# Optimization experiments

Hardware: AMD Instinct MI355X
Metric: run time of the kernel (lower is better)

Reference implementation:

```python
import jax, jax.numpy as jnp
import numpy as np
from jax import lax

EPS = 1e-5

def _conv(x, w, stride=1, pad=0, groups=1):
    return lax.conv_general_dilated(
        x, w, (stride, stride), ((pad, pad), (pad, pad)),
        dimension_numbers=('NCHW', 'OIHW', 'NCHW'),
        feature_group_count=groups)

def _bn(x, gamma, beta):
    # BatchNorm2d, training-mode batch statistics (biased variance)
    mean = jnp.mean(x, axis=(0, 2, 3), keepdims=True)
    var = jnp.var(x, axis=(0, 2, 3), keepdims=True)
    xn = (x - mean) * lax.rsqrt(var + EPS)
    return xn * gamma[None, :, None, None] + beta[None, :, None, None]

def _silu(x):
    return x * jax.nn.sigmoid(x)

def setup_inputs() -> dict:
    key = jax.random.key(0)
    ks = jax.random.split(key, 20)
    B, C, H, W = 16, 128, 128, 128
    L2 = 100
    s = 0.05
    d = {
        'x': jax.random.normal(ks[0], (B, C, H, W), jnp.float32),
        'dce_output': jax.random.normal(ks[1], (B, L2, C), jnp.float32),
        # per-channel 3x3 convs fused as one depthwise conv [C,1,3,3]
        'dw_conv': jax.random.normal(ks[2], (C, 1, 3, 3), jnp.float32) * s,
        'W_dce1': jax.random.normal(ks[3], (L2 * C, C), jnp.float32) * s,
        'b_dce1': jnp.zeros((C,), jnp.float32),
        'W_dce2': jax.random.normal(ks[4], (C, C), jnp.float32) * s,
        'b_dce2': jnp.zeros((C,), jnp.float32),
        'W_sh': jax.random.normal(ks[5], (C, C // 2), jnp.float32) * s,
        'b_sh': jnp.zeros((C // 2,), jnp.float32),
        'W_ex': jax.random.normal(ks[6], (C // 2, C), jnp.float32) * s,
        'b_ex': jnp.zeros((C,), jnp.float32),
        'conv1_w': jax.random.normal(ks[7], (C, C, 3, 3), jnp.float32) * s,
        'bn1_g': jnp.ones((C,), jnp.float32),
        'bn1_b': jnp.zeros((C,), jnp.float32),
        'conv2_w': jax.random.normal(ks[8], (C, C, 1, 1), jnp.float32) * s,
        'bn2_g': jnp.ones((C,), jnp.float32),
        'bn2_b': jnp.zeros((C,), jnp.float32),
        'sc_w': jax.random.normal(ks[9], (C, C, 1, 1), jnp.float32) * s,
        'bnsc_g': jnp.ones((C,), jnp.float32),
        'bnsc_b': jnp.zeros((C,), jnp.float32),
    }
    return d

def reference(x, dce_output, dw_conv, W_dce1, b_dce1, W_dce2, b_dce2,
              W_sh, b_sh, W_ex, b_ex, conv1_w, bn1_g, bn1_b,
              conv2_w, bn2_g, bn2_b, sc_w, bnsc_g, bnsc_b):
    B, C, H, W = x.shape
    stride = 1
    # DCE FFN: Linear -> GELU(exact) -> Linear
    dce_flat = dce_output.reshape(B, -1)
    h = jax.nn.gelu(dce_flat @ W_dce1 + b_dce1, approximate=False)
    dce_features = h @ W_dce2 + b_dce2  # [B, C]
    # per-channel 3x3 conv + global avg pool, fused as depthwise conv
    sp = _conv(x, dw_conv, stride=1, pad=1, groups=C)
    spatial_features = jnp.mean(sp, axis=(2, 3))  # [B, C]
    # SE-style modulation
    m = dce_features * spatial_features
    shrunk = jax.nn.gelu(m @ W_sh + b_sh, approximate=False)
    mod_w = jax.nn.sigmoid(shrunk @ W_ex + b_ex)  # [B, C]
    xm = x * mod_w[:, :, None, None]
    # ResBlock
    bb = _bn(_conv(xm, conv1_w, stride=stride, pad=1), bn1_g, bn1_b)
    bb = _silu(bb)
    bb = _bn(_conv(bb, conv2_w, stride=1, pad=0), bn2_g, bn2_b)
    sc = _bn(_conv(xm, sc_w, stride=stride, pad=0), bnsc_g, bnsc_b)
    return _silu(bb + sc)
```

## Files before the change

kernel.cpp:

```cpp
#include <hip/hip_runtime.h>
#include <hip/hip_bf16.h>

typedef _Float16 f16;
typedef __attribute__((ext_vector_type(8))) _Float16 f16x8;
typedef __attribute__((ext_vector_type(4))) _Float16 f16x4;
typedef __attribute__((ext_vector_type(4))) float f32x4;

__device__ __forceinline__ float geluf(float x) {
    return 0.5f * x * (1.0f + erff(x * 0.70710678118654752440f));
}
__device__ __forceinline__ float sigmf(float x) { return 1.0f / (1.0f + __expf(-x)); }

#define NB 16
#define NC 128
#define NH 128
#define NW 128
#define PLANE (NH * NW)
#define NSTAT 262144.0f

__device__ __align__(16) f16 g_Wc[9 * 4 * 128 * 32];
__device__ __align__(16) f16 g_Wsc[4 * 128 * 32];
__device__ __align__(16) f16 g_W2[4 * 128 * 32];
__device__ __align__(16) f16 g_xmT[(size_t)16 * 128 * 4 * 130 * 32];
__device__ __align__(16) f16 g_y1T[(size_t)16 * 128 * 4 * 128 * 32];
__device__ __align__(16) f16 g_bbT[(size_t)16 * 128 * 4 * 128 * 32];

__global__ __launch_bounds__(256) void k_wprep(const float* __restrict__ c1w,
                                               const float* __restrict__ scw,
                                               const float* __restrict__ c2w) {
    int i = blockIdx.x * 256 + threadIdx.x;
    if (i < 147456) {
        int tap = i / 16384;
        int rem = i - tap * 16384;
        int chunk = rem >> 12;
        int r2 = rem & 4095;
        int co = r2 >> 5;
        int cil = r2 & 31;
        int ci = chunk * 32 + cil;
        g_Wc[i] = (f16)c1w[((size_t)co * 128 + ci) * 9 + tap];
    } else if (i < 163840) {
        int j = i - 147456;
        int chunk = j >> 12;
        int r2 = j & 4095;
        int co = r2 >> 5;
        int cil = r2 & 31;
        g_Wsc[j] = (f16)scw[(size_t)co * 128 + chunk * 32 + cil];
    } else if (i < 180224) {
        int j = i - 163840;
        int chunk = j >> 12;
        int r2 = j & 4095;
        int co = r2 >> 5;
        int cil = j & 31;
        g_W2[j] = (f16)c2w[(size_t)co * 128 + chunk * 32 + cil];
    }
}

__global__ __launch_bounds__(256) void k_dce1(const float* __restrict__ dce,
                                              const float* __restrict__ W1,
                                              float* __restrict__ dh) {
    int ks = blockIdx.x;
    int kbase = ks * 100;
    int t = threadIdx.x;
    __shared__ float sdce[16][100];
    for (int e = t; e < 1600; e += 256) {
        int bb = e / 100, k = e - bb * 100;
        sdce[bb][k] = dce[(size_t)bb * 12800 + kbase + k];
    }
    __syncthreads();
    int j = t & 127;
    int bg = t >> 7;
    float accs[8];
#pragma unroll
    for (int i = 0; i < 8; ++i) accs[i] = 0.0f;
    for (int k = 0; k < 100; ++k) {
        float wv = W1[((size_t)(kbase + k)) * 128 + j];
#pragma unroll
        for (int bb = 0; bb < 8; ++bb) accs[bb] += sdce[bg * 8 + bb][k] * wv;
    }
#pragma unroll
    for (int bb = 0; bb < 8; ++bb)
        atomicAdd(&dh[(bg * 8 + bb) * 128 + j], accs[bb]);
}

__global__ __launch_bounds__(128) void k_dce2(const float* __restrict__ dh,
                                              const float* __restrict__ b1,
                                              const float* __restrict__ W2,
                                              const float* __restrict__ b2,
                                              float* __restrict__ feat) {
    int b = blockIdx.x, j = threadIdx.x;
    __shared__ float sh[128];
    sh[j] = geluf(dh[b * 128 + j] + b1[j]);
    __syncthreads();
    float acc = b2[j];
    for (int k = 0; k < 128; ++k) acc += sh[k] * W2[k * 128 + j];
    feat[b * 128 + j] = acc;
}

__global__ __launch_bounds__(256) void k_spatial(const float* __restrict__ x,
                                                 const float* __restrict__ dw,
                                                 float* __restrict__ spat) {
    int bc = blockIdx.x;
    int t = threadIdx.x;
    const float* p = x + (size_t)bc * PLANE;
    float f = 0, r0 = 0, r1 = 0, c0 = 0, c1 = 0;
    for (int i = t; i < PLANE; i += 256) {
        float v = p[i];
        int row = i >> 7, col = i & 127;
        f += v;
        if (row == 0) r0 += v;
        if (row == 127) r1 += v;
        if (col == 0) c0 += v;
        if (col == 127) c1 += v;
    }
#pragma unroll
    for (int o = 1; o < 64; o <<= 1) {
        f  += __shfl_xor(f, o);
        r0 += __shfl_xor(r0, o);
        r1 += __shfl_xor(r1, o);
        c0 += __shfl_xor(c0, o);
        c1 += __shfl_xor(c1, o);
    }
    __shared__ float wr[4][5];
    int wid = t >> 6;
    if ((t & 63) == 0) {
        wr[wid][0] = f; wr[wid][1] = r0; wr[wid][2] = r1; wr[wid][3] = c0; wr[wid][4] = c1;
    }
    __syncthreads();
    if (t == 0) {
        float full = 0, row0 = 0, row127 = 0, col0 = 0, col127 = 0;
#pragma unroll
        for (int w = 0; w < 4; ++w) {
            full += wr[w][0]; row0 += wr[w][1]; row127 += wr[w][2];
            col0 += wr[w][3]; col127 += wr[w][4];
        }
        int c = bc & 127;
        float x00 = p[0];
        float x0e = p[127];
        float xe0 = p[127 * 128];
        float xee = p[127 * 128 + 127];
        float acc = 0.0f;
        for (int kh = 0; kh < 3; ++kh)
            for (int kw = 0; kw < 3; ++kw) {
                int dh_ = kh - 1, dwv = kw - 1;
                float T = full;
                if (dh_ == -1) T -= row127;
                else if (dh_ == 1) T -= row0;
                if (dwv == -1) T -= col127;
                else if (dwv == 1) T -= col0;
                if (dh_ == -1 && dwv == -1) T += xee;
                if (dh_ == -1 && dwv == 1) T += xe0;
                if (dh_ == 1 && dwv == -1) T += x0e;
                if (dh_ == 1 && dwv == 1) T += x00;
                acc += dw[c * 9 + kh * 3 + kw] * T;
            }
        spat[bc] = acc * (1.0f / 16384.0f);
    }
}

__global__ __launch_bounds__(128) void k_mod(const float* __restrict__ feat,
                                             const float* __restrict__ spat,
                                             const float* __restrict__ Wsh,
                                             const float* __restrict__ bsh,
                                             const float* __restrict__ Wex,
                                             const float* __restrict__ bex,
                                             float* __restrict__ mod) {
    int b = blockIdx.x, t = threadIdx.x;
    __shared__ float sm[128], ssh[64];
    sm[t] = feat[b * 128 + t] * spat[b * 128 + t];
    __syncthreads();
    if (t < 64) {
        float acc = bsh[t];
        for (int c = 0; c < 128; ++c) acc += sm[c] * Wsh[c * 64 + t];
        ssh[t] = geluf(acc);
    }
    __syncthreads();
    float acc = bex[t];
    for (int k = 0; k < 64; ++k) acc += ssh[k] * Wex[k * 128 + t];
    mod[b * 128 + t] = sigmf(acc);
}

__global__ __launch_bounds__(256) void k_xprep(const float* __restrict__ x,
                                               const float* __restrict__ mod) {
    int bid = blockIdx.x;
    int h = bid & 127;
    int b = bid >> 7;
    int t = threadIdx.x;
    __shared__ float sx[32][133];

    for (int chunk = 0; chunk < 4; ++chunk) {
        __syncthreads();
#pragma unroll
        for (int it = 0; it < 4; ++it) {
            int ci = it * 8 + (t >> 5);
            int w4 = t & 31;
            int cig = chunk * 32 + ci;
            float4 v = *(const float4*)&x[(((size_t)b * 128 + cig) * 128 + h) * 128 + w4 * 4];
            float m = mod[b * 128 + cig];
            sx[ci][w4 * 4 + 0] = v.x * m;
            sx[ci][w4 * 4 + 1] = v.y * m;
            sx[ci][w4 * 4 + 2] = v.z * m;
            sx[ci][w4 * 4 + 3] = v.w * m;
        }
        __syncthreads();
        f16* dstc = g_xmT + (((size_t)(b * 128 + h)) * 4 + chunk) * 4160;
        for (int g = t; g < 520; g += 256) {
            int s = g >> 2, c8 = g & 3;
            f16x8 o;
            if (s == 0 || s == 129) {
#pragma unroll
                for (int j = 0; j < 8; ++j) o[j] = (f16)0.f;
            } else {
#pragma unroll
                for (int j = 0; j < 8; ++j) o[j] = (f16)sx[c8 * 8 + j][s - 1];
            }
            *(f16x8*)(dstc + s * 32 + c8 * 8) = o;
        }
    }
}

__global__ __launch_bounds__(256, 3) void k_conv1m(float* __restrict__ stats) {
    int orig = blockIdx.x;
    int sw = (orig & 7) * 256 + (orig >> 3);
    int h = sw & 127;
    int b = sw >> 7;
    int t = threadIdx.x;
    int lane = t & 63;
    int wv = t >> 6;
    int l15 = lane & 15, lg = lane >> 4;
    int co_half = (wv >> 1) * 64;
    int w_half = (wv & 1) * 64;

    f32x4 acc[4][4];
#pragma unroll
    for (int ct = 0; ct < 4; ++ct)
#pragma unroll
        for (int wt = 0; wt < 4; ++wt) acc[ct][wt] = (f32x4){0.f, 0.f, 0.f, 0.f};

    f16x8 z8;
#pragma unroll
    for (int j = 0; j < 8; ++j) z8[j] = (f16)0.f;

    const f16* xrow[3];
    bool rok[3];
#pragma unroll
    for (int r = 0; r < 3; ++r) {
        int hr = h + r - 1;
        rok[r] = ((unsigned)hr < 128u);
        xrow[r] = g_xmT + ((size_t)(b * 128 + (rok[r] ? hr : 0))) * 4 * 4160;
    }

#pragma unroll
    for (int chunk = 0; chunk < 4; ++chunk) {
#pragma unroll
        for (int tap = 0; tap < 9; ++tap) {
            const int kh = tap / 3, kw = tap - kh * 3;
            f16x8 af[4], bf[4];
#pragma unroll
            for (int ct = 0; ct < 4; ++ct)
                af[ct] = *(const f16x8*)(g_Wc + ((size_t)(tap * 4 + chunk) * 128 + co_half + ct * 16 + l15) * 32 + lg * 8);
            if (rok[kh]) {
#pragma unroll
                for (int wt = 0; wt < 4; ++wt)
                    bf[wt] = *(const f16x8*)(xrow[kh] + (size_t)chunk * 4160
                                             + (w_half + wt * 16 + l15 + kw) * 32 + lg * 8);
            } else {
#pragma unroll
                for (int wt = 0; wt < 4; ++wt) bf[wt] = z8;
            }
#pragma unroll
            for (int ct = 0; ct < 4; ++ct)
#pragma unroll
                for (int wt = 0; wt < 4; ++wt)
                    acc[ct][wt] = __builtin_amdgcn_mfma_f32_16x16x32_f16(
                        af[ct], bf[wt], acc[ct][wt], 0, 0, 0);
        }
    }

#pragma unroll
    for (int ct = 0; ct < 4; ++ct) {
        int cog = (wv >> 1) * 2 + (ct >> 1);
        int col = (ct & 1) * 16 + lg * 4;
#pragma unroll
        for (int wt = 0; wt < 4; ++wt) {
            int w = w_half + wt * 16 + l15;
            f16x4 pk;
            pk[0] = (f16)acc[ct][wt][0];
            pk[1] = (f16)acc[ct][wt][1];
            pk[2] = (f16)acc[ct][wt][2];
            pk[3] = (f16)acc[ct][wt][3];
            *(f16x4*)(g_y1T + ((((size_t)(b * 128 + h)) * 4 + cog) * 128 + w) * 32 + col) = pk;
        }
#pragma unroll
        for (int r = 0; r < 4; ++r) {
            int co = co_half + ct * 16 + lg * 4 + r;
            float s = 0, q = 0;
#pragma unroll
            for (int wt = 0; wt < 4; ++wt) {
                float v = acc[ct][wt][r];
                s += v; q += v * v;
            }
#pragma unroll
            for (int o = 1; o < 16; o <<= 1) {
                s += __shfl_xor(s, o);
                q += __shfl_xor(q, o);
            }
            if (l15 == 0) {
                atomicAdd(&stats[co], s);
                atomicAdd(&stats[128 + co], q);
            }
        }
    }
}

__global__ __launch_bounds__(128) void k_fin1(const float* __restrict__ stats,
                                              const float* __restrict__ g1, const float* __restrict__ be1,
                                              float* __restrict__ coef) {
    int t = threadIdx.x;
    const float inv = 1.0f / NSTAT;
    float m = stats[t] * inv;
    float v = stats[128 + t] * inv - m * m;
    float a = g1[t] * rsqrtf(v + 1e-5f);
    coef[t] = a;
    coef[128 + t] = be1[t] - m * a;
}

__global__ __launch_bounds__(256, 2) void k_conv2m(const float* __restrict__ coef,
                                                   float* __restrict__ stats) {
    int orig = blockIdx.x;
    int sw = (orig & 7) * 256 + (orig >> 3);
    int h = sw & 127;
    int b = sw >> 7;
    int t = threadIdx.x;
    int lane = t & 63;
    int wv = t >> 6;
    int l15 = lane & 15, lg = lane >> 4;
    int co_half = (wv >> 1) * 64;
    int w_half = (wv & 1) * 64;

    f32x4 acc[4][4], asc[4][4];
#pragma unroll
    for (int ct = 0; ct < 4; ++ct)
#pragma unroll
        for (int wt = 0; wt < 4; ++wt) {
            acc[ct][wt] = (f32x4){0.f, 0.f, 0.f, 0.f};
            asc[ct][wt] = (f32x4){0.f, 0.f, 0.f, 0.f};
        }

    for (int chunk = 0; chunk < 4; ++chunk) {
        float ca[8], cc[8];
#pragma unroll
        for (int j = 0; j < 8; ++j) {
            int ci = chunk * 32 + lg * 8 + j;
            ca[j] = coef[ci];
            cc[j] = coef[128 + ci];
        }
        f16x8 bfr[4], bx[4];
#pragma unroll
        for (int wt = 0; wt < 4; ++wt) {
            int w = w_half + wt * 16 + l15;
            f16x8 raw = *(const f16x8*)(g_y1T + ((((size_t)(b * 128 + h)) * 4 + chunk) * 128 + w) * 32 + lg * 8);
#pragma unroll
            for (int j = 0; j < 8; ++j) {
                float v = ca[j] * (float)raw[j] + cc[j];
                bfr[wt][j] = (f16)(v * sigmf(v));
            }
            bx[wt] = *(const f16x8*)(g_xmT + (((size_t)(b * 128 + h)) * 4 + chunk) * 4160 + (w + 1) * 32 + lg * 8);
        }
        if (wv < 2) {
#pragma unroll
            for (int wt = 0; wt < 4; ++wt) {
                int w = w_half + wt * 16 + l15;
                *(f16x8*)(g_bbT + ((((size_t)(b * 128 + h)) * 4 + chunk) * 128 + w) * 32 + lg * 8) = bfr[wt];
            }
        }
        f16x8 af[4], sf[4];
#pragma unroll
        for (int ct = 0; ct < 4; ++ct) {
            af[ct] = *(const f16x8*)(g_W2 + ((size_t)chunk * 128 + co_half + ct * 16 + l15) * 32 + lg * 8);
            sf[ct] = *(const f16x8*)(g_Wsc + ((size_t)chunk * 128 + co_half + ct * 16 + l15) * 32 + lg * 8);
        }
#pragma unroll
        for (int ct = 0; ct < 4; ++ct)
#pragma unroll
            for (int wt = 0; wt < 4; ++wt) {
                acc[ct][wt] = __builtin_amdgcn_mfma_f32_16x16x32_f16(
                    af[ct], bfr[wt], acc[ct][wt], 0, 0, 0);
                asc[ct][wt] = __builtin_amdgcn_mfma_f32_16x16x32_f16(
                    sf[ct], bx[wt], asc[ct][wt], 0, 0, 0);
            }
    }

#pragma unroll
    for (int ct = 0; ct < 4; ++ct) {
#pragma unroll
        for (int r = 0; r < 4; ++r) {
            int co = co_half + ct * 16 + lg * 4 + r;
            float s = 0, q = 0, ss = 0, qq = 0;
#pragma unroll
            for (int wt = 0; wt < 4; ++wt) {
                float v = acc[ct][wt][r];
                s += v; q += v * v;
                float u = asc[ct][wt][r];
                ss += u; qq += u * u;
            }
#pragma unroll
            for (int o = 1; o < 16; o <<= 1) {
                s += __shfl_xor(s, o);
                q += __shfl_xor(q, o);
                ss += __shfl_xor(ss, o);
                qq += __shfl_xor(qq, o);
            }
            if (l15 == 0) {
                atomicAdd(&stats[512 + co], s);
                atomicAdd(&stats[640 + co], q);
                atomicAdd(&stats[256 + co], ss);
                atomicAdd(&stats[384 + co], qq);
            }
        }
    }
}

__global__ __launch_bounds__(256) void k_fin2(const float* __restrict__ stats,
                                              const float* __restrict__ g2, const float* __restrict__ be2,
                                              const float* __restrict__ gsc, const float* __restrict__ bsc,
                                              float* __restrict__ coef) {
    int t = threadIdx.x;
    const float inv = 1.0f / NSTAT;
    if (t < 128) {
        float m = stats[512 + t] * inv;
        float v = stats[640 + t] * inv - m * m;
        float a = g2[t] * rsqrtf(v + 1e-5f);
        coef[512 + t] = a;
        coef[640 + t] = be2[t] - m * a;
    } else {
        int c = t - 128;
        float m = stats[256 + c] * inv;
        float v = stats[384 + c] * inv - m * m;
        float a = gsc[c] * rsqrtf(v + 1e-5f);
        coef[256 + c] = a;
        coef[384 + c] = bsc[c] - m * a;
    }
}

__global__ __launch_bounds__(256, 2) void k_final(float* __restrict__ out,
                                                  const float* __restrict__ coef) {
    int orig = blockIdx.x;
    int sw = (orig & 7) * 256 + (orig >> 3);
    int h = sw & 127;
    int b = sw >> 7;
    int t = threadIdx.x;
    int lane = t & 63;
    int wv = t >> 6;
    int l15 = lane & 15, lg = lane >> 4;
    int co_half = (wv >> 1) * 64;
    int w_half = (wv & 1) * 64;

    f32x4 acc[4][4], asc[4][4];
#pragma unroll
    for (int ct = 0; ct < 4; ++ct)
#pragma unroll
        for (int wt = 0; wt < 4; ++wt) {
            acc[ct][wt] = (f32x4){0.f, 0.f, 0.f, 0.f};
            asc[ct][wt] = (f32x4){0.f, 0.f, 0.f, 0.f};
        }

    for (int chunk = 0; chunk < 4; ++chunk) {
        f16x8 bf[4], bx[4], af[4], sf[4];
#pragma unroll
        for (int wt = 0; wt < 4; ++wt) {
            int w = w_half + wt * 16 + l15;
            bf[wt] = *(const f16x8*)(g_bbT + ((((size_t)(b * 128 + h)) * 4 + chunk) * 128 + w) * 32 + lg * 8);
            bx[wt] = *(const f16x8*)(g_xmT + (((size_t)(b * 128 + h)) * 4 + chunk) * 4160 + (w + 1) * 32 + lg * 8);
        }
#pragma unroll
        for (int ct = 0; ct < 4; ++ct) {
            af[ct] = *(const f16x8*)(g_W2 + ((size_t)chunk * 128 + co_half + ct * 16 + l15) * 32 + lg * 8);
            sf[ct] = *(const f16x8*)(g_Wsc + ((size_t)chunk * 128 + co_half + ct * 16 + l15) * 32 + lg * 8);
        }
#pragma unroll
        for (int ct = 0; ct < 4; ++ct)
#pragma unroll
            for (int wt = 0; wt < 4; ++wt) {
                acc[ct][wt] = __builtin_amdgcn_mfma_f32_16x16x32_f16(
                    af[ct], bf[wt], acc[ct][wt], 0, 0, 0);
                asc[ct][wt] = __builtin_amdgcn_mfma_f32_16x16x32_f16(
                    sf[ct], bx[wt], asc[ct][wt], 0, 0, 0);
            }
    }

#pragma unroll
    for (int ct = 0; ct < 4; ++ct) {
#pragma unroll
        for (int r = 0; r < 4; ++r) {
            int co = co_half + ct * 16 + lg * 4 + r;
            float a2 = coef[512 + co], c2 = coef[640 + co];
            float as = coef[256 + co], cs = coef[384 + co];
#pragma unroll
            for (int wt = 0; wt < 4; ++wt) {
                float v = a2 * acc[ct][wt][r] + c2 + as * asc[ct][wt][r] + cs;
                v = v * sigmf(v);
                out[(((size_t)b * 128 + co) * 128 + h) * 128 + w_half + wt * 16 + l15] = v;
            }
        }
    }
}

extern "C" void kernel_launch(void* const* d_in, const int* in_sizes, int n_in,
                              void* d_out, int out_size, void* d_ws, size_t ws_size,
                              hipStream_t stream) {
    (void)in_sizes; (void)n_in; (void)out_size; (void)ws_size;
    const float* x    = (const float*)d_in[0];
    const float* dce  = (const float*)d_in[1];
    const float* dwc  = (const float*)d_in[2];
    const float* W1   = (const float*)d_in[3];
    const float* b1   = (const float*)d_in[4];
    const float* W2d  = (const float*)d_in[5];
    const float* b2d  = (const float*)d_in[6];
    const float* Wsh  = (const float*)d_in[7];
    const float* bsh  = (const float*)d_in[8];
    const float* Wex  = (const float*)d_in[9];
    const float* bex  = (const float*)d_in[10];
    const float* c1w  = (const float*)d_in[11];
    const float* g1   = (const float*)d_in[12];
    const float* be1  = (const float*)d_in[13];
    const float* c2w  = (const float*)d_in[14];
    const float* g2   = (const float*)d_in[15];
    const float* be2  = (const float*)d_in[16];
    const float* scw  = (const float*)d_in[17];
    const float* gsc  = (const float*)d_in[18];
    const float* bsc  = (const float*)d_in[19];

    float* F = (float*)d_ws;
    float* dh    = F;
    float* stats = F + 2048;
    float* coef  = F + 2816;
    float* feat  = F + 3584;
    float* spat  = F + 5632;
    float* md    = F + 7680;

    float* out = (float*)d_out;

    hipMemsetAsync(F, 0, (2048 + 768) * sizeof(float), stream);

    k_wprep<<<704, 256, 0, stream>>>(c1w, scw, c2w);
    k_dce1<<<128, 256, 0, stream>>>(dce, W1, dh);
    k_dce2<<<16, 128, 0, stream>>>(dh, b1, W2d, b2d, feat);
    k_spatial<<<2048, 256, 0, stream>>>(x, dwc, spat);
    k_mod<<<16, 128, 0, stream>>>(feat, spat, Wsh, bsh, Wex, bex, md);
    k_xprep<<<2048, 256, 0, stream>>>(x, md);
    k_conv1m<<<2048, 256, 0, stream>>>(stats);
    k_fin1<<<1, 128, 0, stream>>>(stats, g1, be1, coef);
    k_conv2m<<<2048, 256, 0, stream>>>(coef, stats);
    k_fin2<<<1, 256, 0, stream>>>(stats, g2, be2, gsc, bsc, coef);
    k_final<<<2048, 256, 0, stream>>>(out, coef);
}
```

Baseline: 1.266 ms.

## Fold modulation into per-batch weights, fuse spatial stats into x transpose, LDS-stage conv1

The separate spatial-reduction pass over x is removed; k_xprep now accumulates the per-channel sums, border rows/columns and corners with atomics while it transposes unmodulated x to fp16. The channel modulation is folded into per-batch copies of the conv1 and shortcut weights (k_wmod), so x no longer needs a second modulated pass. conv1 stages its three input rows into double-buffered, swizzled LDS via global_load_lds instead of reading them directly from global memory. conv2 no longer writes bbT and the final kernel recomputes BN+SiLU from y1T, which removes one large intermediate write and read. In exchange there are more atomics, per-batch weight storage, and duplicated elementwise work.

New measurement: 1.288 ms. No clear change (+1.7%).

```diff
diff --git a/kernel.cpp b/kernel.cpp
--- a/kernel.cpp
+++ b/kernel.cpp
@@ -21,14 +21,19 @@
 __device__ __align__(16) f16 g_Wc[9 * 4 * 128 * 32];
 __device__ __align__(16) f16 g_Wsc[4 * 128 * 32];
 __device__ __align__(16) f16 g_W2[4 * 128 * 32];
-__device__ __align__(16) f16 g_xmT[(size_t)16 * 128 * 4 * 130 * 32];
+__device__ __align__(16) f16 g_Wcb[(size_t)16 * 9 * 4 * 128 * 32];
+__device__ __align__(16) f16 g_Wscb[(size_t)16 * 4 * 128 * 32];
+__device__ __align__(16) f16 g_xT[(size_t)16 * 128 * 4 * 130 * 32];
 __device__ __align__(16) f16 g_y1T[(size_t)16 * 128 * 4 * 128 * 32];
-__device__ __align__(16) f16 g_bbT[(size_t)16 * 128 * 4 * 128 * 32];
+__device__ __align__(16) f16 g_zrow[4160];
+__device__ float g_red[5][16][128];
+__device__ float g_corn[4][16][128];
 
 __global__ __launch_bounds__(256) void k_wprep(const float* __restrict__ c1w,
                                                const float* __restrict__ scw,
                                                const float* __restrict__ c2w) {
     int i = blockIdx.x * 256 + threadIdx.x;
+    if (i < 10240) ((float*)g_red)[i] = 0.0f;
     if (i < 147456) {
         int tap = i / 16384;
         int rem = i - tap * 16384;
@@ -96,50 +101,77 @@
     feat[b * 128 + j] = acc;
 }
 
-__global__ __launch_bounds__(256) void k_spatial(const float* __restrict__ x,
-                                                 const float* __restrict__ dw,
-                                                 float* __restrict__ spat) {
-    int bc = blockIdx.x;
-    int t = threadIdx.x;
-    const float* p = x + (size_t)bc * PLANE;
-    float f = 0, r0 = 0, r1 = 0, c0 = 0, c1 = 0;
-    for (int i = t; i < PLANE; i += 256) {
-        float v = p[i];
-        int row = i >> 7, col = i & 127;
-        f += v;
-        if (row == 0) r0 += v;
-        if (row == 127) r1 += v;
-        if (col == 0) c0 += v;
-        if (col == 127) c1 += v;
-    }
-#pragma unroll
-    for (int o = 1; o < 64; o <<= 1) {
-        f  += __shfl_xor(f, o);
-        r0 += __shfl_xor(r0, o);
-        r1 += __shfl_xor(r1, o);
-        c0 += __shfl_xor(c0, o);
-        c1 += __shfl_xor(c1, o);
-    }
-    __shared__ float wr[4][5];
-    int wid = t >> 6;
-    if ((t & 63) == 0) {
-        wr[wid][0] = f; wr[wid][1] = r0; wr[wid][2] = r1; wr[wid][3] = c0; wr[wid][4] = c1;
-    }
-    __syncthreads();
-    if (t == 0) {
-        float full = 0, row0 = 0, row127 = 0, col0 = 0, col127 = 0;
-#pragma unroll
-        for (int w = 0; w < 4; ++w) {
-            full += wr[w][0]; row0 += wr[w][1]; row127 += wr[w][2];
-            col0 += wr[w][3]; col127 += wr[w][4];
-        }
-        int c = bc & 127;
-        float x00 = p[0];
-        float x0e = p[127];
-        float xe0 = p[127 * 128];
-        float xee = p[127 * 128 + 127];
+__global__ __launch_bounds__(256) void k_xprep(const float* __restrict__ x) {
+    int bid = blockIdx.x;
+    int h = bid & 127;
+    int b = bid >> 7;
+    int t = threadIdx.x;
+    int w4 = t & 31;
+    __shared__ float sx[32][133];
+
+    for (int chunk = 0; chunk < 4; ++chunk) {
+        __syncthreads();
+#pragma unroll
+        for (int it = 0; it < 4; ++it) {
+            int ci = it * 8 + (t >> 5);
+            int cig = chunk * 32 + ci;
+            float4 v = *(const float4*)&x[(((size_t)b * 128 + cig) * 128 + h) * 128 + w4 * 4];
+            sx[ci][w4 * 4 + 0] = v.x;
+            sx[ci][w4 * 4 + 1] = v.y;
+            sx[ci][w4 * 4 + 2] = v.z;
+            sx[ci][w4 * 4 + 3] = v.w;
+            float s4 = v.x + v.y + v.z + v.w;
+#pragma unroll
+            for (int o = 1; o < 32; o <<= 1) s4 += __shfl_xor(s4, o);
+            if (w4 == 0) {
+                atomicAdd(&g_red[0][b][cig], s4);
+                if (h == 0) atomicAdd(&g_red[1][b][cig], s4);
+                if (h == 127) atomicAdd(&g_red[2][b][cig], s4);
+                atomicAdd(&g_red[3][b][cig], v.x);
+                if (h == 0) g_corn[0][b][cig] = v.x;
+                if (h == 127) g_corn[2][b][cig] = v.x;
+            }
+            if (w4 == 31) {
+                atomicAdd(&g_red[4][b][cig], v.w);
+                if (h == 0) g_corn[1][b][cig] = v.w;
+                if (h == 127) g_corn[3][b][cig] = v.w;
+            }
+        }
+        __syncthreads();
+        f16* dstc = g_xT + (((size_t)(b * 128 + h)) * 4 + chunk) * 4160;
+        for (int g = t; g < 520; g += 256) {
+            int s = g >> 2, c8 = g & 3;
+            f16x8 o;
+            if (s == 0 || s == 129) {
+#pragma unroll
+                for (int j = 0; j < 8; ++j) o[j] = (f16)0.f;
+            } else {
+#pragma unroll
+                for (int j = 0; j < 8; ++j) o[j] = (f16)sx[c8 * 8 + j][s - 1];
+            }
+            *(f16x8*)(dstc + s * 32 + c8 * 8) = o;
+        }
+    }
+}
+
+__global__ __launch_bounds__(128) void k_mod(const float* __restrict__ feat,
+                                             const float* __restrict__ dw,
+                                             const float* __restrict__ Wsh,
+                                             const float* __restrict__ bsh,
+                                             const float* __restrict__ Wex,
+                                             const float* __restrict__ bex,
+                                             float* __restrict__ mod) {
+    int b = blockIdx.x, t = threadIdx.x;
+    __shared__ float sm[128], ssh[64];
+    {
+        float full = g_red[0][b][t], row0 = g_red[1][b][t], row127 = g_red[2][b][t];
+        float col0 = g_red[3][b][t], col127 = g_red[4][b][t];
+        float x00 = g_corn[0][b][t], x0e = g_corn[1][b][t];
+        float xe0 = g_corn[2][b][t], xee = g_corn[3][b][t];
         float acc = 0.0f;
+#pragma unroll
         for (int kh = 0; kh < 3; ++kh)
+#pragma unroll
             for (int kw = 0; kw < 3; ++kw) {
                 int dh_ = kh - 1, dwv = kw - 1;
                 float T = full;
@@ -151,22 +183,11 @@
                 if (dh_ == -1 && dwv == 1) T += xe0;
                 if (dh_ == 1 && dwv == -1) T += x0e;
                 if (dh_ == 1 && dwv == 1) T += x00;
-                acc += dw[c * 9 + kh * 3 + kw] * T;
-            }
-        spat[bc] = acc * (1.0f / 16384.0f);
-    }
-}
-
-__global__ __launch_bounds__(128) void k_mod(const float* __restrict__ feat,
-                                             const float* __restrict__ spat,
-                                             const float* __restrict__ Wsh,
-                                             const float* __restrict__ bsh,
-                                             const float* __restrict__ Wex,
-                                             const float* __restrict__ bex,
-                                             float* __restrict__ mod) {
-    int b = blockIdx.x, t = threadIdx.x;
-    __shared__ float sm[128], ssh[64];
-    sm[t] = feat[b * 128 + t] * spat[b * 128 + t];
+                acc += dw[t * 9 + kh * 3 + kw] * T;
+            }
+        float spat = acc * (1.0f / 16384.0f);
+        sm[t] = feat[b * 128 + t] * spat;
+    }
     __syncthreads();
     if (t < 64) {
         float acc = bsh[t];
@@ -179,42 +200,21 @@
     mod[b * 128 + t] = sigmf(acc);
 }
 
-__global__ __launch_bounds__(256) void k_xprep(const float* __restrict__ x,
-                                               const float* __restrict__ mod) {
-    int bid = blockIdx.x;
-    int h = bid & 127;
-    int b = bid >> 7;
-    int t = threadIdx.x;
-    __shared__ float sx[32][133];
-
-    for (int chunk = 0; chunk < 4; ++chunk) {
-        __syncthreads();
-#pragma unroll
-        for (int it = 0; it < 4; ++it) {
-            int ci = it * 8 + (t >> 5);
-            int w4 = t & 31;
-            int cig = chunk * 32 + ci;
-            float4 v = *(const float4*)&x[(((size_t)b * 128 + cig) * 128 + h) * 128 + w4 * 4];
-            float m = mod[b * 128 + cig];
-            sx[ci][w4 * 4 + 0] = v.x * m;
-            sx[ci][w4 * 4 + 1] = v.y * m;
-            sx[ci][w4 * 4 + 2] = v.z * m;
-            sx[ci][w4 * 4 + 3] = v.w * m;
-        }
-        __syncthreads();
-        f16* dstc = g_xmT + (((size_t)(b * 128 + h)) * 4 + chunk) * 4160;
-        for (int g = t; g < 520; g += 256) {
-            int s = g >> 2, c8 = g & 3;
-            f16x8 o;
-            if (s == 0 || s == 129) {
-#pragma unroll
-                for (int j = 0; j < 8; ++j) o[j] = (f16)0.f;
-            } else {
-#pragma unroll
-                for (int j = 0; j < 8; ++j) o[j] = (f16)sx[c8 * 8 + j][s - 1];
-            }
-            *(f16x8*)(dstc + s * 32 + c8 * 8) = o;
-        }
+__global__ __launch_bounds__(256) void k_wmod(const float* __restrict__ mod) {
+    int i = blockIdx.x * 256 + threadIdx.x;
+    if (i < 2359296) {
+        int b = i / 147456;
+        int rem = i - b * 147456;
+        int chunk = (rem >> 12) & 3;
+        int cil = rem & 31;
+        g_Wcb[i] = (f16)((float)g_Wc[rem] * mod[b * 128 + chunk * 32 + cil]);
+    } else if (i < 2621440) {
+        int j = i - 2359296;
+        int b = j / 16384;
+        int rem = j - b * 16384;
+        int chunk = rem >> 12;
+        int cil = rem & 31;
+        g_Wscb[j] = (f16)((float)g_Wsc[rem] * mod[b * 128 + chunk * 32 + cil]);
     }
 }
 
@@ -230,42 +230,59 @@
     int co_half = (wv >> 1) * 64;
     int w_half = (wv & 1) * 64;
 
+    __shared__ __align__(16) f16 xs[2][3][130][32];
+
     f32x4 acc[4][4];
 #pragma unroll
     for (int ct = 0; ct < 4; ++ct)
 #pragma unroll
         for (int wt = 0; wt < 4; ++wt) acc[ct][wt] = (f32x4){0.f, 0.f, 0.f, 0.f};
 
-    f16x8 z8;
-#pragma unroll
-    for (int j = 0; j < 8; ++j) z8[j] = (f16)0.f;
-
-    const f16* xrow[3];
-    bool rok[3];
+    const f16* rowc[3];
 #pragma unroll
     for (int r = 0; r < 3; ++r) {
         int hr = h + r - 1;
-        rok[r] = ((unsigned)hr < 128u);
-        xrow[r] = g_xmT + ((size_t)(b * 128 + (rok[r] ? hr : 0))) * 4 * 4160;
-    }
-
-#pragma unroll
-    for (int chunk = 0; chunk < 4; ++chunk) {
+        rowc[r] = ((unsigned)hr < 128u) ? (g_xT + ((size_t)(b * 128 + hr)) * 4 * 4160)
+                                        : (const f16*)0;
+    }
+
+    auto stage = [&](int c, int u) {
+#pragma unroll
+        for (int i = 0; i < 7; ++i) {
+            int g = t + i * 256;
+            if (g < 1560) {
+                int r = g / 520;
+                int p = g - r * 520;
+                int q = (p & ~3) | ((p & 3) ^ ((p >> 3) & 3));
+                const f16* src = rowc[r] ? (rowc[r] + c * 4160 + q * 8) : (g_zrow + q * 8);
+                f16* dst = &xs[u][0][0][0] + (size_t)g * 8;
+                __builtin_amdgcn_global_load_lds(
+                    (const __attribute__((address_space(1))) unsigned int*)src,
+                    (__attribute__((address_space(3))) unsigned int*)dst, 16, 0, 0);
+            }
+        }
+    };
+
+    stage(0, 0);
+    __syncthreads();
+
+#pragma unroll
+    for (int c = 0; c < 4; ++c) {
+        const int u = c & 1;
+        if (c < 3) stage(c + 1, u ^ 1);
+
 #pragma unroll
         for (int tap = 0; tap < 9; ++tap) {
             const int kh = tap / 3, kw = tap - kh * 3;
             f16x8 af[4], bf[4];
 #pragma unroll
             for (int ct = 0; ct < 4; ++ct)
-                af[ct] = *(const f16x8*)(g_Wc + ((size_t)(tap * 4 + chunk) * 128 + co_half + ct * 16 + l15) * 32 + lg * 8);
-            if (rok[kh]) {
-#pragma unroll
-                for (int wt = 0; wt < 4; ++wt)
-                    bf[wt] = *(const f16x8*)(xrow[kh] + (size_t)chunk * 4160
-                                             + (w_half + wt * 16 + l15 + kw) * 32 + lg * 8);
-            } else {
-#pragma unroll
-                for (int wt = 0; wt < 4; ++wt) bf[wt] = z8;
+                af[ct] = *(const f16x8*)(g_Wcb + ((((size_t)b * 9 + tap) * 4 + c) * 128
+                                                  + co_half + ct * 16 + l15) * 32 + lg * 8);
+#pragma unroll
+            for (int wt = 0; wt < 4; ++wt) {
+                int s = w_half + wt * 16 + l15 + kw;
+                bf[wt] = *(const f16x8*)&xs[u][kh][s][(lg ^ ((s >> 1) & 3)) * 8];
             }
 #pragma unroll
             for (int ct = 0; ct < 4; ++ct)
@@ -274,6 +291,7 @@
                     acc[ct][wt] = __builtin_amdgcn_mfma_f32_16x16x32_f16(
                         af[ct], bf[wt], acc[ct][wt], 0, 0, 0);
         }
+        __syncthreads();
     }
 
 #pragma unroll
@@ -346,6 +364,7 @@
             asc[ct][wt] = (f32x4){0.f, 0.f, 0.f, 0.f};
         }
 
+#pragma unroll
     for (int chunk = 0; chunk < 4; ++chunk) {
         float ca[8], cc[8];
 #pragma unroll
@@ -364,20 +383,13 @@
                 float v = ca[j] * (float)raw[j] + cc[j];
                 bfr[wt][j] = (f16)(v * sigmf(v));
             }
-            bx[wt] = *(const f16x8*)(g_xmT + (((size_t)(b * 128 + h)) * 4 + chunk) * 4160 + (w + 1) * 32 + lg * 8);
-        }
-        if (wv < 2) {
-#pragma unroll
-            for (int wt = 0; wt < 4; ++wt) {
-                int w = w_half + wt * 16 + l15;
-                *(f16x8*)(g_bbT + ((((size_t)(b * 128 + h)) * 4 + chunk) * 128 + w) * 32 + lg * 8) = bfr[wt];
-            }
+            bx[wt] = *(const f16x8*)(g_xT + (((size_t)(b * 128 + h)) * 4 + chunk) * 4160 + (w + 1) * 32 + lg * 8);
         }
         f16x8 af[4], sf[4];
 #pragma unroll
         for (int ct = 0; ct < 4; ++ct) {
             af[ct] = *(const f16x8*)(g_W2 + ((size_t)chunk * 128 + co_half + ct * 16 + l15) * 32 + lg * 8);
-            sf[ct] = *(const f16x8*)(g_Wsc + ((size_t)chunk * 128 + co_half + ct * 16 + l15) * 32 + lg * 8);
+            sf[ct] = *(const f16x8*)(g_Wscb + (((size_t)b * 4 + chunk) * 128 + co_half + ct * 16 + l15) * 32 + lg * 8);
         }
 #pragma unroll
         for (int ct = 0; ct < 4; ++ct)
@@ -464,18 +476,31 @@
             asc[ct][wt] = (f32x4){0.f, 0.f, 0.f, 0.f};
         }
 
+#pragma unroll
     for (int chunk = 0; chunk < 4; ++chunk) {
+        float ca[8], cc[8];
+#pragma unroll
+        for (int j = 0; j < 8; ++j) {
+            int ci = chunk * 32 + lg * 8 + j;
+            ca[j] = coef[ci];
+            cc[j] = coef[128 + ci];
+        }
         f16x8 bf[4], bx[4], af[4], sf[4];
 #pragma unroll
         for (int wt = 0; wt < 4; ++wt) {
             int w = w_half + wt * 16 + l15;
-            bf[wt] = *(const f16x8*)(g_bbT + ((((size_t)(b * 128 + h)) * 4 + chunk) * 128 + w) * 32 + lg * 8);
-            bx[wt] = *(const f16x8*)(g_xmT + (((size_t)(b * 128 + h)) * 4 + chunk) * 4160 + (w + 1) * 32 + lg * 8);
+            f16x8 raw = *(const f16x8*)(g_y1T + ((((size_t)(b * 128 + h)) * 4 + chunk) * 128 + w) * 32 + lg * 8);
+#pragma unroll
+            for (int j = 0; j < 8; ++j) {
+                float v = ca[j] * (float)raw[j] + cc[j];
+                bf[wt][j] = (f16)(v * sigmf(v));
+            }
+            bx[wt] = *(const f16x8*)(g_xT + (((size_t)(b * 128 + h)) * 4 + chunk) * 4160 + (w + 1) * 32 + lg * 8);
         }
 #pragma unroll
         for (int ct = 0; ct < 4; ++ct) {
             af[ct] = *(const f16x8*)(g_W2 + ((size_t)chunk * 128 + co_half + ct * 16 + l15) * 32 + lg * 8);
-            sf[ct] = *(const f16x8*)(g_Wsc + ((size_t)chunk * 128 + co_half + ct * 16 + l15) * 32 + lg * 8);
+            sf[ct] = *(const f16x8*)(g_Wscb + (((size_t)b * 4 + chunk) * 128 + co_half + ct * 16 + l15) * 32 + lg * 8);
         }
 #pragma unroll
         for (int ct = 0; ct < 4; ++ct)
@@ -535,19 +560,18 @@
     float* stats = F + 2048;
     float* coef  = F + 2816;
     float* feat  = F + 3584;
-    float* spat  = F + 5632;
-    float* md    = F + 7680;
+    float* md    = F + 5632;
 
     float* out = (float*)d_out;
 
-    hipMemsetAsync(F, 0, (2048 + 768) * sizeof(float), stream);
+    hipMemsetAsync(F, 0, 2816 * sizeof(float), stream);
 
     k_wprep<<<704, 256, 0, stream>>>(c1w, scw, c2w);
     k_dce1<<<128, 256, 0, stream>>>(dce, W1, dh);
     k_dce2<<<16, 128, 0, stream>>>(dh, b1, W2d, b2d, feat);
-    k_spatial<<<2048, 256, 0, stream>>>(x, dwc, spat);
-    k_mod<<<16, 128, 0, stream>>>(feat, spat, Wsh, bsh, Wex, bex, md);
-    k_xprep<<<2048, 256, 0, stream>>>(x, md);
+    k_xprep<<<2048, 256, 0, stream>>>(x);
+    k_mod<<<16, 128, 0, stream>>>(feat, dwc, Wsh, bsh, Wex, bex, md);
+    k_wmod<<<10240, 256, 0, stream>>>(md);
     k_conv1m<<<2048, 256, 0, stream>>>(stats);
     k_fin1<<<1, 128, 0, stream>>>(stats, g1, be1, coef);
     k_conv2m<<<2048, 256, 0, stream>>>(coef, stats);
```
